# Kernel tuning notes

Measured on AMD Instinct MI355X. Metric: run time of the kernel, lower is better.

The kernel has to match this reference:

```python
import jax, jax.numpy as jnp
import numpy as np

N_NODES = 500_000
MEM_D = 128
MSG_D = 256  # stored messages have MSG_D + 1 columns (message + timestamp slot)
B = 200_000


def setup_inputs() -> dict:
    key = jax.random.key(0)
    k1, k2, k3, k4, k5, k6, k7 = jax.random.split(key, 7)
    memory = jax.random.normal(k1, (N_NODES, MEM_D), dtype=jnp.float32)
    last_update = jax.random.uniform(k2, (N_NODES,), dtype=jnp.float32)
    messages = jax.random.normal(k3, (N_NODES, MSG_D + 1), dtype=jnp.float32)
    node_id_to_messages = jax.random.normal(k4, (N_NODES, MSG_D + 1), dtype=jnp.float32)
    values = jax.random.normal(k5, (B, MEM_D), dtype=jnp.float32)
    node_idxs = jax.random.randint(k6, (B,), 0, N_NODES, dtype=jnp.int64 if jax.config.jax_enable_x64 else jnp.int32)
    nodes = jax.random.randint(k7, (B,), 0, N_NODES, dtype=jnp.int64 if jax.config.jax_enable_x64 else jnp.int32)
    return {
        "memory": memory,
        "last_update": last_update,
        "messages": messages,
        "node_id_to_messages": node_id_to_messages,
        "values": values,
        "node_idxs": node_idxs,
        "nodes": nodes,
    }


def reference(memory, last_update, messages, node_id_to_messages, values, node_idxs, nodes):
    # get_memory: row gather from persistent memory buffer
    mem_out = memory[node_idxs]                      # [B, MEM_D]
    # get_last_update: scalar gather
    lu_out = last_update[node_idxs]                  # [B]
    # set_memory: row scatter (index_copy) into memory buffer
    new_memory = memory.at[node_idxs].set(values)    # [N, MEM_D]
    # store_raw_messages: messages[nodes, :] = node_id_to_messages[nodes]
    new_messages = messages.at[nodes].set(node_id_to_messages[nodes])  # [N, MSG_D+1]
    return mem_out, lu_out, new_memory, new_messages
```

## Files before the change

### kernel.cpp

```cpp
#include <hip/hip_runtime.h>

#define N_NODES 500000
#define MEM_D   128
#define MSG_W   257
#define BATCH   200000


__global__ void scatter_idx_kernel(const int* __restrict__ node_idxs,
                                   const int* __restrict__ nodes,
                                   int* __restrict__ winner,
                                   unsigned char* __restrict__ flag) {
    int i = blockIdx.x * blockDim.x + threadIdx.x;
    int stride = gridDim.x * blockDim.x;
    for (; i < BATCH; i += stride) {
        atomicMax(&winner[node_idxs[i]], i);
        flag[nodes[i]] = 1;
    }
}

__global__ void gather_kernel(const float* __restrict__ memory,
                              const float* __restrict__ last_update,
                              const int* __restrict__ node_idxs,
                              float* __restrict__ mem_out,
                              float* __restrict__ lu_out) {
    const long total = (long)BATCH * (MEM_D / 4);
    long i = (long)blockIdx.x * blockDim.x + threadIdx.x;
    long stride = (long)gridDim.x * blockDim.x;
    const float4* mem4 = reinterpret_cast<const float4*>(memory);
    float4* out4 = reinterpret_cast<float4*>(mem_out);
    for (; i < total; i += stride) {
        int row  = (int)(i >> 5);
        int col4 = (int)(i & 31);
        int idx  = node_idxs[row];
        out4[i] = mem4[(long)idx * 32 + col4];
        if (col4 == 0) lu_out[row] = last_update[idx];
    }
}

__global__ void setmem_kernel(const float* __restrict__ memory,
                              const float* __restrict__ values,
                              const int* __restrict__ winner,
                              float* __restrict__ new_memory) {
    const long total = (long)N_NODES * (MEM_D / 4);
    long i = (long)blockIdx.x * blockDim.x + threadIdx.x;
    long stride = (long)gridDim.x * blockDim.x;
    const float4* mem4 = reinterpret_cast<const float4*>(memory);
    const float4* val4 = reinterpret_cast<const float4*>(values);
    float4* out4 = reinterpret_cast<float4*>(new_memory);
    for (; i < total; i += stride) {
        int row  = (int)(i >> 5);
        int col4 = (int)(i & 31);
        int w = winner[row];
        float4 v;
        if (w >= 0) {
            v = val4[(long)w * 32 + col4];
        } else {
            v = mem4[i];
        }
        out4[i] = v;
    }
}

__global__ void setmsg_kernel(const float* __restrict__ messages,
                              const float* __restrict__ src,
                              const unsigned char* __restrict__ flag,
                              float* __restrict__ out) {
    const int total4 = (N_NODES / 4) * MSG_W;
    int i = blockIdx.x * blockDim.x + threadIdx.x;
    int stride = gridDim.x * blockDim.x;
    const float4* m4 = reinterpret_cast<const float4*>(messages);
    const float4* s4 = reinterpret_cast<const float4*>(src);
    float4* o4 = reinterpret_cast<float4*>(out);
    for (; i < total4; i += stride) {
        int e  = i * 4;
        int r0 = e / 257;
        int r3 = (e + 3) / 257;
        if (r0 == r3) {
            float4 v;
            if (flag[r0]) {
                v = s4[i];
            } else {
                v = m4[i];
            }
            o4[i] = v;
        } else {
            #pragma unroll
            for (int k = 0; k < 4; ++k) {
                int r = (e + k) / 257;
                float v;
                if (flag[r]) {
                    v = src[e + k];
                } else {
                    v = messages[e + k];
                }
                out[e + k] = v;
            }
        }
    }
}

extern "C" void kernel_launch(void* const* d_in, const int* in_sizes, int n_in,
                              void* d_out, int out_size, void* d_ws, size_t ws_size,
                              hipStream_t stream) {
    const float* memory       = (const float*)d_in[0];
    const float* last_update  = (const float*)d_in[1];
    const float* messages     = (const float*)d_in[2];
    const float* nid2msg      = (const float*)d_in[3];
    const float* values       = (const float*)d_in[4];
    const int*   node_idxs    = (const int*)d_in[5];
    const int*   nodes        = (const int*)d_in[6];

    float* out = (float*)d_out;
    float* mem_out      = out;
    float* lu_out       = out + (long)BATCH * MEM_D;
    float* new_memory   = lu_out + BATCH;
    float* new_messages = new_memory + (long)N_NODES * MEM_D;

    int* winner = (int*)d_ws;
    unsigned char* flag = (unsigned char*)d_ws + (size_t)N_NODES * sizeof(int);

    hipMemsetAsync(winner, 0xFF, (size_t)N_NODES * sizeof(int), stream);
    hipMemsetAsync(flag, 0, (size_t)N_NODES, stream);

    const int BS = 256;

    scatter_idx_kernel<<<(BATCH + BS - 1) / BS, BS, 0, stream>>>(
        node_idxs, nodes, winner, flag);

    gather_kernel<<<2048, BS, 0, stream>>>(memory, last_update, node_idxs,
                                           mem_out, lu_out);
    setmem_kernel<<<2048, BS, 0, stream>>>(memory, values, winner, new_memory);
    setmsg_kernel<<<2048, BS, 0, stream>>>(messages, nid2msg, flag, new_messages);
}
```

Baseline: 388.8 us.

## Fuse gather, memory scatter and message copy into one streaming kernel

```diff
diff --git a/kernel.cpp b/kernel.cpp
--- a/kernel.cpp
+++ b/kernel.cpp
@@ -5,6 +5,28 @@
 #define MSG_W   257
 #define BATCH   200000
 
+#define G_UNITS   6400000
+#define M_UNITS   16000000
+#define S_UNITS   32125000
+#define GM_UNITS  22400000
+#define TOTAL_UNITS 54525000
+
+typedef float f4 __attribute__((ext_vector_type(4)));
+
+__device__ __forceinline__ f4 nt_load4(const f4* p) {
+    return __builtin_nontemporal_load(p);
+}
+__device__ __forceinline__ void nt_store4(f4* p, f4 v) {
+    __builtin_nontemporal_store(v, p);
+}
+
+__global__ void init_kernel(int* __restrict__ winner,
+                            unsigned int* __restrict__ flag32) {
+    int i = blockIdx.x * blockDim.x + threadIdx.x;
+    int stride = gridDim.x * blockDim.x;
+    for (int j = i; j < N_NODES; j += stride) winner[j] = -1;
+    for (int j = i; j < N_NODES / 4; j += stride) flag32[j] = 0u;
+}
 
 __global__ void scatter_idx_kernel(const int* __restrict__ node_idxs,
                                    const int* __restrict__ nodes,
@@ -18,82 +40,70 @@
     }
 }
 
-__global__ void gather_kernel(const float* __restrict__ memory,
-                              const float* __restrict__ last_update,
-                              const int* __restrict__ node_idxs,
-                              float* __restrict__ mem_out,
-                              float* __restrict__ lu_out) {
-    const long total = (long)BATCH * (MEM_D / 4);
-    long i = (long)blockIdx.x * blockDim.x + threadIdx.x;
-    long stride = (long)gridDim.x * blockDim.x;
-    const float4* mem4 = reinterpret_cast<const float4*>(memory);
-    float4* out4 = reinterpret_cast<float4*>(mem_out);
-    for (; i < total; i += stride) {
-        int row  = (int)(i >> 5);
-        int col4 = (int)(i & 31);
-        int idx  = node_idxs[row];
-        out4[i] = mem4[(long)idx * 32 + col4];
-        if (col4 == 0) lu_out[row] = last_update[idx];
-    }
-}
+__global__ void fused_kernel(const float* __restrict__ memory,
+                             const float* __restrict__ last_update,
+                             const float* __restrict__ messages,
+                             const float* __restrict__ nid2msg,
+                             const float* __restrict__ values,
+                             const int* __restrict__ node_idxs,
+                             const int* __restrict__ winner,
+                             const unsigned char* __restrict__ flag,
+                             float* __restrict__ mem_out,
+                             float* __restrict__ lu_out,
+                             float* __restrict__ new_memory,
+                             float* __restrict__ new_messages) {
+    const f4* mem4 = reinterpret_cast<const f4*>(memory);
+    const f4* val4 = reinterpret_cast<const f4*>(values);
+    const f4* msg4 = reinterpret_cast<const f4*>(messages);
+    const f4* src4 = reinterpret_cast<const f4*>(nid2msg);
+    f4* memout4 = reinterpret_cast<f4*>(mem_out);
+    f4* newmem4 = reinterpret_cast<f4*>(new_memory);
+    f4* newmsg4 = reinterpret_cast<f4*>(new_messages);
 
-__global__ void setmem_kernel(const float* __restrict__ memory,
-                              const float* __restrict__ values,
-                              const int* __restrict__ winner,
-                              float* __restrict__ new_memory) {
-    const long total = (long)N_NODES * (MEM_D / 4);
-    long i = (long)blockIdx.x * blockDim.x + threadIdx.x;
-    long stride = (long)gridDim.x * blockDim.x;
-    const float4* mem4 = reinterpret_cast<const float4*>(memory);
-    const float4* val4 = reinterpret_cast<const float4*>(values);
-    float4* out4 = reinterpret_cast<float4*>(new_memory);
-    for (; i < total; i += stride) {
-        int row  = (int)(i >> 5);
-        int col4 = (int)(i & 31);
-        int w = winner[row];
-        float4 v;
-        if (w >= 0) {
-            v = val4[(long)w * 32 + col4];
-        } else {
-            v = mem4[i];
-        }
-        out4[i] = v;
-    }
-}
-
-__global__ void setmsg_kernel(const float* __restrict__ messages,
-                              const float* __restrict__ src,
-                              const unsigned char* __restrict__ flag,
-                              float* __restrict__ out) {
-    const int total4 = (N_NODES / 4) * MSG_W;
     int i = blockIdx.x * blockDim.x + threadIdx.x;
     int stride = gridDim.x * blockDim.x;
-    const float4* m4 = reinterpret_cast<const float4*>(messages);
-    const float4* s4 = reinterpret_cast<const float4*>(src);
-    float4* o4 = reinterpret_cast<float4*>(out);
-    for (; i < total4; i += stride) {
-        int e  = i * 4;
-        int r0 = e / 257;
-        int r3 = (e + 3) / 257;
-        if (r0 == r3) {
-            float4 v;
-            if (flag[r0]) {
-                v = s4[i];
+    for (; i < TOTAL_UNITS; i += stride) {
+        if (i < G_UNITS) {
+            int row  = i >> 5;
+            int col4 = i & 31;
+            int idx  = node_idxs[row];
+            f4 v = mem4[(long)idx * 32 + col4];
+            nt_store4(&memout4[i], v);
+            if (col4 == 0) {
+                __builtin_nontemporal_store(last_update[idx], &lu_out[row]);
+            }
+        } else if (i < GM_UNITS) {
+            int j    = i - G_UNITS;
+            int row  = j >> 5;
+            int col4 = j & 31;
+            int w = winner[row];
+            f4 v;
+            if (w >= 0) {
+                v = val4[(long)w * 32 + col4];
             } else {
-                v = m4[i];
+                v = nt_load4(&mem4[j]);
             }
-            o4[i] = v;
+            nt_store4(&newmem4[j], v);
         } else {
-            #pragma unroll
-            for (int k = 0; k < 4; ++k) {
-                int r = (e + k) / 257;
-                float v;
-                if (flag[r]) {
-                    v = src[e + k];
+            int j = i - GM_UNITS;
+            int e  = j * 4;
+            int r0 = e / 257;
+            int r3 = (e + 3) / 257;
+            if (r0 == r3) {
+                f4 v;
+                if (flag[r0]) {
+                    v = nt_load4(&src4[j]);
                 } else {
-                    v = messages[e + k];
+                    v = nt_load4(&msg4[j]);
                 }
-                out[e + k] = v;
+                nt_store4(&newmsg4[j], v);
+            } else {
+                #pragma unroll
+                for (int k = 0; k < 4; ++k) {
+                    int r = (e + k) / 257;
+                    float v = (flag[r] ? nid2msg : messages)[e + k];
+                    new_messages[e + k] = v;
+                }
             }
         }
     }
@@ -119,16 +129,16 @@
     int* winner = (int*)d_ws;
     unsigned char* flag = (unsigned char*)d_ws + (size_t)N_NODES * sizeof(int);
 
-    hipMemsetAsync(winner, 0xFF, (size_t)N_NODES * sizeof(int), stream);
-    hipMemsetAsync(flag, 0, (size_t)N_NODES, stream);
+    const int BS = 256;
 
-    const int BS = 256;
+    init_kernel<<<512, BS, 0, stream>>>(winner, (unsigned int*)flag);
 
     scatter_idx_kernel<<<(BATCH + BS - 1) / BS, BS, 0, stream>>>(
         node_idxs, nodes, winner, flag);
 
-    gather_kernel<<<2048, BS, 0, stream>>>(memory, last_update, node_idxs,
-                                           mem_out, lu_out);
-    setmem_kernel<<<2048, BS, 0, stream>>>(memory, values, winner, new_memory);
-    setmsg_kernel<<<2048, BS, 0, stream>>>(messages, nid2msg, flag, new_messages);
+    fused_kernel<<<2048, BS, 0, stream>>>(memory, last_update, messages,
+                                          nid2msg, values, node_idxs,
+                                          winner, flag,
+                                          mem_out, lu_out, new_memory,
+                                          new_messages);
 }
```

Measured after the change: 360.7 us. 7.2% less time.
